# Optimization experiments

Hardware: AMD Instinct MI355X
Metric: run time of the kernel (lower is better)

Reference implementation:

```python
import jax, jax.numpy as jnp
import numpy as np


def setup_inputs() -> dict:
    key = jax.random.key(0)
    k1, k2, k3, k4, k5 = jax.random.split(key, 5)
    B, S, I, N = 64, 512, 2, 2048
    scale = (1.0 / N) ** 0.5
    velocities = jax.random.normal(k1, (B, S, I), dtype=jnp.float32)
    h0 = jax.random.uniform(k2, (B, N), dtype=jnp.float32)
    W_lin = jax.random.normal(k3, (N, I), dtype=jnp.float32) * scale
    b_lin = jax.random.normal(k4, (N,), dtype=jnp.float32) * scale
    W_rec = jax.random.normal(k5, (N, N), dtype=jnp.float32) * scale
    return {"velocities": velocities, "h0": h0, "W_lin": W_lin,
            "b_lin": b_lin, "W_rec": W_rec}


def reference(velocities, h0, W_lin, b_lin, W_rec):
    # velocities: [B, S, 2]; h0: [B, N]; W_lin: [N, 2]; b_lin: [N]; W_rec: [N, N]
    # base_logits = Linear(velocities): [B, S, N]
    base_logits = jnp.einsum('bsi,ni->bsn', velocities, W_lin) + b_lin

    def step(h, logits_t):
        # logits_t: [B, N]; h: [B, N] (probabilities)
        z = logits_t + h @ W_rec
        h_new = jax.nn.softmax(z, axis=-1)
        return h_new, h_new

    # scan over time axis S
    _, outs = jax.lax.scan(step, h0, jnp.swapaxes(base_logits, 0, 1))
    # outs: [S, B, N] -> [B, S, N]
    return jnp.swapaxes(outs, 0, 1)
```

## Files before the change

### kernel.cpp

```cpp
#include <hip/hip_runtime.h>
#include <stdint.h>

typedef __attribute__((ext_vector_type(8))) short short8;
typedef __attribute__((ext_vector_type(4))) float floatx4;

static constexpr int kB = 64, kS = 512, kN = 2048;

static constexpr size_t CTR_OFF        = 0;
static constexpr size_t CTR_BYTES      = 4 * 513 * 4;
static constexpr size_t RSP_OFF        = 16384;
static constexpr size_t RSP_BYTES_BIG  = (size_t)kS * 4 * 16 * 64 * 4;
static constexpr size_t RSP_BYTES_SM   = (size_t)2 * 4 * 16 * 64 * 4;
static constexpr size_t SLAB           = (size_t)kB * kN * 2;
static constexpr size_t EBUF_OFF_BIG   = RSP_OFF + RSP_BYTES_BIG;
static constexpr size_t TOTAL_BIG      = EBUF_OFF_BIG + 513 * SLAB;
static constexpr size_t EBUF_OFF_SM    = RSP_OFF + RSP_BYTES_SM;
static constexpr size_t TOTAL_SM       = EBUF_OFF_SM + 2 * SLAB;

__device__ __forceinline__ unsigned short f2bf(float x) {
    unsigned u = __builtin_bit_cast(unsigned, x);
    u = (u + 0x7fffu + ((u >> 16) & 1u)) >> 16;
    return (unsigned short)u;
}

__device__ __forceinline__ void domain_barrier(unsigned* slot, unsigned count) {
    __syncthreads();
    if (threadIdx.x == 0) {
        __hip_atomic_fetch_add(slot, 1u, __ATOMIC_RELAXED, __HIP_MEMORY_SCOPE_AGENT);
        while (__hip_atomic_load(slot, __ATOMIC_RELAXED, __HIP_MEMORY_SCOPE_AGENT) < count)
            __builtin_amdgcn_s_sleep(1);
    }
    __syncthreads();
}

struct ULL2 { unsigned long long lo, hi; };

template<bool BIG>
__global__ __launch_bounds__(256) void pcn(
    const float* __restrict__ vel, const float* __restrict__ h0,
    const float* __restrict__ Wlin, const float* __restrict__ blin,
    const float* __restrict__ Wrec, float* __restrict__ out,
    float* rsp, unsigned* ctr, unsigned short* ebuf)
{
    extern __shared__ char smem[];
    short8* Wlds = (short8*)smem;
    float*  red  = (float*)(smem + 131072);

    const int tid  = threadIdx.x;
    const int lane = tid & 63;
    const int w    = tid >> 6;
    const int bg   = (blockIdx.x & 7) >> 1;
    const int cg   = ((blockIdx.x >> 3) << 1) | (blockIdx.x & 1);
    const int b0   = bg * 16;
    const int c0   = cg * 32;
    const int koff = (lane >> 4) << 3;

    for (int kt = w * 16; kt < w * 16 + 16; ++kt) {
        for (int ct = 0; ct < 2; ++ct) {
            const int colg = c0 + ct * 16 + (lane & 15);
            const int kb   = kt * 32 + koff;
            short8 v;
            #pragma unroll
            for (int j = 0; j < 8; ++j)
                v[j] = (short)f2bf(Wrec[(size_t)(kb + j) * kN + colg]);
            Wlds[(kt * 2 + ct) * 64 + lane] = v;
        }
    }

    const int r   = tid >> 4;
    const int c16 = tid & 15;
    const int cc  = c16 * 2;

    {
        const float a0 = h0[(size_t)(b0 + r) * kN + c0 + cc];
        const float a1 = h0[(size_t)(b0 + r) * kN + c0 + cc + 1];
        const unsigned pk = (unsigned)f2bf(a0) | ((unsigned)f2bf(a1) << 16);
        __hip_atomic_store((unsigned*)(ebuf + (size_t)(b0 + r) * kN + c0 + cc), pk,
                           __ATOMIC_RELAXED, __HIP_MEMORY_SCOPE_AGENT);
    }

    const float wl00 = Wlin[(c0 + cc) * 2 + 0],     wl01 = Wlin[(c0 + cc) * 2 + 1];
    const float wl10 = Wlin[(c0 + cc + 1) * 2 + 0], wl11 = Wlin[(c0 + cc + 1) * 2 + 1];
    const float bl0  = blin[c0 + cc], bl1 = blin[c0 + cc + 1];

    domain_barrier(ctr + bg * 513 + 512, 64);

    float s_inv = 1.0f;
    float ep0 = 0.0f, ep1 = 0.0f;
    const int arow = b0 + (lane & 15);

    for (int t = 0; t < kS; ++t) {
        const int rslot = BIG ? t       : (t & 1);
        const int wslot = BIG ? (t + 1) : ((t + 1) & 1);
        const unsigned short* ebR = ebuf + (size_t)rslot * (kB * kN);

        floatx4 acc0 = {0.f,0.f,0.f,0.f}, acc1 = {0.f,0.f,0.f,0.f};
        #pragma unroll
        for (int kt = 0; kt < 16; ++kt) {
            const int ktg = w * 16 + kt;
            const unsigned short* ap = ebR + (size_t)arow * kN + ktg * 32 + koff;
            short8 a;
            if (BIG) {
                a = *(const short8*)ap;
            } else {
                ULL2 u;
                u.lo = __hip_atomic_load((const unsigned long long*)ap,
                                         __ATOMIC_RELAXED, __HIP_MEMORY_SCOPE_AGENT);
                u.hi = __hip_atomic_load((const unsigned long long*)ap + 1,
                                         __ATOMIC_RELAXED, __HIP_MEMORY_SCOPE_AGENT);
                a = __builtin_bit_cast(short8, u);
            }
            const short8 bq0 = Wlds[(ktg * 2 + 0) * 64 + lane];
            const short8 bq1 = Wlds[(ktg * 2 + 1) * 64 + lane];
            acc0 = __builtin_amdgcn_mfma_f32_16x16x32_bf16(a, bq0, acc0, 0, 0, 0);
            acc1 = __builtin_amdgcn_mfma_f32_16x16x32_bf16(a, bq1, acc1, 0, 0, 0);
        }
        {
            const int ccol = lane & 15, crow = (lane >> 4) * 4;
            #pragma unroll
            for (int i = 0; i < 4; ++i) {
                red[w * 512 + (crow + i) * 32 + ccol]      = acc0[i];
                red[w * 512 + (crow + i) * 32 + 16 + ccol] = acc1[i];
            }
        }
        __syncthreads();
        float g0 = 0.f, g1 = 0.f;
        {
            const int cell = tid * 2;
            #pragma unroll
            for (int ww = 0; ww < 4; ++ww) {
                g0 += red[ww * 512 + cell];
                g1 += red[ww * 512 + cell + 1];
            }
        }

        const float v0 = vel[((size_t)(b0 + r) * kS + t) * 2 + 0];
        const float v1 = vel[((size_t)(b0 + r) * kS + t) * 2 + 1];
        const float z0 = fmaf(g0, s_inv, fmaf(v0, wl00, fmaf(v1, wl01, bl0)));
        const float z1 = fmaf(g1, s_inv, fmaf(v0, wl10, fmaf(v1, wl11, bl1)));
        const float e0 = __expf(z0), e1 = __expf(z1);

        float es = e0 + e1;
        es += __shfl_xor(es, 8, 16);
        es += __shfl_xor(es, 4, 16);
        es += __shfl_xor(es, 2, 16);
        es += __shfl_xor(es, 1, 16);
        if (c16 == 0) {
            const size_t pidx = (((size_t)rslot * 4 + bg) * 16 + r) * 64 + cg;
            __hip_atomic_store(rsp + pidx, es, __ATOMIC_RELAXED, __HIP_MEMORY_SCOPE_AGENT);
        }

        {
            const unsigned pk = (unsigned)f2bf(e0) | ((unsigned)f2bf(e1) << 16);
            __hip_atomic_store(
                (unsigned*)(ebuf + (size_t)wslot * (kB * kN) + (size_t)(b0 + r) * kN + c0 + cc),
                pk, __ATOMIC_RELAXED, __HIP_MEMORY_SCOPE_AGENT);
        }

        if (t > 0) {
            float2 o; o.x = ep0 * s_inv; o.y = ep1 * s_inv;
            *(float2*)(out + ((size_t)(b0 + r) * kS + (t - 1)) * kN + c0 + cc) = o;
        }
        ep0 = e0; ep1 = e1;

        domain_barrier(ctr + bg * 513 + t, 64);

        {
            const float* rp = rsp + (((size_t)rslot * 4 + bg) * 16 + r) * 64 + c16 * 4;
            float s;
            if (BIG) {
                const floatx4 v = *(const floatx4*)rp;
                s = (v[0] + v[1]) + (v[2] + v[3]);
            } else {
                float p0 = __hip_atomic_load(rp + 0, __ATOMIC_RELAXED, __HIP_MEMORY_SCOPE_AGENT);
                float p1 = __hip_atomic_load(rp + 1, __ATOMIC_RELAXED, __HIP_MEMORY_SCOPE_AGENT);
                float p2 = __hip_atomic_load(rp + 2, __ATOMIC_RELAXED, __HIP_MEMORY_SCOPE_AGENT);
                float p3 = __hip_atomic_load(rp + 3, __ATOMIC_RELAXED, __HIP_MEMORY_SCOPE_AGENT);
                s = (p0 + p1) + (p2 + p3);
            }
            s += __shfl_xor(s, 8, 16);
            s += __shfl_xor(s, 4, 16);
            s += __shfl_xor(s, 2, 16);
            s += __shfl_xor(s, 1, 16);
            s_inv = 1.0f / s;
        }
    }
    {
        float2 o; o.x = ep0 * s_inv; o.y = ep1 * s_inv;
        *(float2*)(out + ((size_t)(b0 + r) * kS + (kS - 1)) * kN + c0 + cc) = o;
    }
}

extern "C" void kernel_launch(void* const* d_in, const int* in_sizes, int n_in,
                              void* d_out, int out_size, void* d_ws, size_t ws_size,
                              hipStream_t stream)
{
    (void)in_sizes; (void)n_in; (void)out_size;
    const float* vel  = (const float*)d_in[0];
    const float* h0   = (const float*)d_in[1];
    const float* Wlin = (const float*)d_in[2];
    const float* blin = (const float*)d_in[3];
    const float* Wrec = (const float*)d_in[4];
    float* out = (float*)d_out;

    char* ws = (char*)d_ws;
    unsigned* ctr = (unsigned*)(ws + CTR_OFF);
    const bool big = ws_size >= TOTAL_BIG;
    float* rsp            = (float*)(ws + RSP_OFF);
    unsigned short* ebuf  = (unsigned short*)(ws + (big ? EBUF_OFF_BIG : EBUF_OFF_SM));

    (void)hipMemsetAsync(ws + CTR_OFF, 0, CTR_BYTES, stream);

    const unsigned smem = 131072 + 8192;
    const void* fn = big ? (const void*)pcn<true> : (const void*)pcn<false>;
    (void)hipFuncSetAttribute(fn, hipFuncAttributeMaxDynamicSharedMemorySize, (int)smem);

    void* args[] = { (void*)&vel, (void*)&h0, (void*)&Wlin, (void*)&blin,
                     (void*)&Wrec, (void*)&out, (void*)&rsp, (void*)&ctr, (void*)&ebuf };
    hipError_t err = hipLaunchCooperativeKernel(fn, dim3(256), dim3(256), args, smem, stream);
    if (err != hipSuccess) {
        (void)hipGetLastError();
        if (big)
            hipLaunchKernelGGL(pcn<true>, dim3(256), dim3(256), smem, stream,
                               vel, h0, Wlin, blin, Wrec, out, rsp, ctr, ebuf);
        else
            hipLaunchKernelGGL(pcn<false>, dim3(256), dim3(256), smem, stream,
                               vel, h0, Wlin, blin, Wrec, out, rsp, ctr, ebuf);
    }
}
```

Measured before the change: 2.716 ms.

## Replace counter barrier with per-block flagged partial sums and a ring buffer

Drops the atomic counter barrier (fetch-add followed by a single-thread spin) and instead has each block publish its nonzero partial softmax sum as a flag. Every thread polls all 64 partials directly, which merges synchronisation and the normaliser reduction into one step. The exp buffer becomes a 4-slot ring, all A-fragment loads are issued before the MFMA loop, and each step's output is written in the same iteration instead of one step later. The risks are more polling traffic from all threads, correctness that depends on relaxed ordering between the ebuf stores and the flag stores, and a zero-sum flag being read as not ready.

```diff
diff --git a/kernel.cpp b/kernel.cpp
--- a/kernel.cpp
+++ b/kernel.cpp
@@ -5,17 +5,12 @@
 typedef __attribute__((ext_vector_type(4))) float floatx4;
 
 static constexpr int kB = 64, kS = 512, kN = 2048;
-
-static constexpr size_t CTR_OFF        = 0;
-static constexpr size_t CTR_BYTES      = 4 * 513 * 4;
-static constexpr size_t RSP_OFF        = 16384;
-static constexpr size_t RSP_BYTES_BIG  = (size_t)kS * 4 * 16 * 64 * 4;
-static constexpr size_t RSP_BYTES_SM   = (size_t)2 * 4 * 16 * 64 * 4;
-static constexpr size_t SLAB           = (size_t)kB * kN * 2;
-static constexpr size_t EBUF_OFF_BIG   = RSP_OFF + RSP_BYTES_BIG;
-static constexpr size_t TOTAL_BIG      = EBUF_OFF_BIG + 513 * SLAB;
-static constexpr size_t EBUF_OFF_SM    = RSP_OFF + RSP_BYTES_SM;
-static constexpr size_t TOTAL_SM       = EBUF_OFF_SM + 2 * SLAB;
+static constexpr int RING = 4;
+
+static constexpr size_t FLG_OFF    = 0;
+static constexpr size_t FLG_BYTES  = (size_t)(kS + 1) * 4 * 64 * 16 * 4;
+static constexpr size_t EBUF_OFF   = (FLG_BYTES + 4095) & ~(size_t)4095;
+static constexpr size_t SLAB_ELEMS = (size_t)kB * kN;
 
 __device__ __forceinline__ unsigned short f2bf(float x) {
     unsigned u = __builtin_bit_cast(unsigned, x);
@@ -23,24 +18,13 @@
     return (unsigned short)u;
 }
 
-__device__ __forceinline__ void domain_barrier(unsigned* slot, unsigned count) {
-    __syncthreads();
-    if (threadIdx.x == 0) {
-        __hip_atomic_fetch_add(slot, 1u, __ATOMIC_RELAXED, __HIP_MEMORY_SCOPE_AGENT);
-        while (__hip_atomic_load(slot, __ATOMIC_RELAXED, __HIP_MEMORY_SCOPE_AGENT) < count)
-            __builtin_amdgcn_s_sleep(1);
-    }
-    __syncthreads();
-}
-
 struct ULL2 { unsigned long long lo, hi; };
 
-template<bool BIG>
 __global__ __launch_bounds__(256) void pcn(
     const float* __restrict__ vel, const float* __restrict__ h0,
     const float* __restrict__ Wlin, const float* __restrict__ blin,
     const float* __restrict__ Wrec, float* __restrict__ out,
-    float* rsp, unsigned* ctr, unsigned short* ebuf)
+    float* flg, unsigned short* ebuf)
 {
     extern __shared__ char smem[];
     short8* Wlds = (short8*)smem;
@@ -83,33 +67,43 @@
     const float wl10 = Wlin[(c0 + cc + 1) * 2 + 0], wl11 = Wlin[(c0 + cc + 1) * 2 + 1];
     const float bl0  = blin[c0 + cc], bl1 = blin[c0 + cc + 1];
 
-    domain_barrier(ctr + bg * 513 + 512, 64);
+    __syncthreads();
+    if (c16 == 0)
+        __hip_atomic_store(flg + (((size_t)kS * 4 + bg) * 64 + cg) * 16 + r, 1.0f,
+                           __ATOMIC_RELAXED, __HIP_MEMORY_SCOPE_AGENT);
+    {
+        const float* fpb = flg + ((size_t)kS * 4 + bg) * 64 * 16 + r;
+        bool rdy = false;
+        do {
+            const float p0 = __hip_atomic_load(fpb + (c16 * 4 + 0) * 16, __ATOMIC_RELAXED, __HIP_MEMORY_SCOPE_AGENT);
+            const float p1 = __hip_atomic_load(fpb + (c16 * 4 + 1) * 16, __ATOMIC_RELAXED, __HIP_MEMORY_SCOPE_AGENT);
+            const float p2 = __hip_atomic_load(fpb + (c16 * 4 + 2) * 16, __ATOMIC_RELAXED, __HIP_MEMORY_SCOPE_AGENT);
+            const float p3 = __hip_atomic_load(fpb + (c16 * 4 + 3) * 16, __ATOMIC_RELAXED, __HIP_MEMORY_SCOPE_AGENT);
+            rdy = (p0 != 0.f) & (p1 != 0.f) & (p2 != 0.f) & (p3 != 0.f);
+        } while (!__all((int)rdy));
+    }
 
     float s_inv = 1.0f;
-    float ep0 = 0.0f, ep1 = 0.0f;
     const int arow = b0 + (lane & 15);
 
     for (int t = 0; t < kS; ++t) {
-        const int rslot = BIG ? t       : (t & 1);
-        const int wslot = BIG ? (t + 1) : ((t + 1) & 1);
-        const unsigned short* ebR = ebuf + (size_t)rslot * (kB * kN);
-
+        const float2 vv = *(const float2*)(vel + ((size_t)(b0 + r) * kS + t) * 2);
+
+        const unsigned short* ebR = ebuf + (size_t)(t % RING) * SLAB_ELEMS;
+        ULL2 afrag[16];
+        #pragma unroll
+        for (int kt = 0; kt < 16; ++kt) {
+            const int ktg = w * 16 + kt;
+            const unsigned long long* ap =
+                (const unsigned long long*)(ebR + (size_t)arow * kN + ktg * 32 + koff);
+            afrag[kt].lo = __hip_atomic_load(ap,     __ATOMIC_RELAXED, __HIP_MEMORY_SCOPE_AGENT);
+            afrag[kt].hi = __hip_atomic_load(ap + 1, __ATOMIC_RELAXED, __HIP_MEMORY_SCOPE_AGENT);
+        }
         floatx4 acc0 = {0.f,0.f,0.f,0.f}, acc1 = {0.f,0.f,0.f,0.f};
         #pragma unroll
         for (int kt = 0; kt < 16; ++kt) {
             const int ktg = w * 16 + kt;
-            const unsigned short* ap = ebR + (size_t)arow * kN + ktg * 32 + koff;
-            short8 a;
-            if (BIG) {
-                a = *(const short8*)ap;
-            } else {
-                ULL2 u;
-                u.lo = __hip_atomic_load((const unsigned long long*)ap,
-                                         __ATOMIC_RELAXED, __HIP_MEMORY_SCOPE_AGENT);
-                u.hi = __hip_atomic_load((const unsigned long long*)ap + 1,
-                                         __ATOMIC_RELAXED, __HIP_MEMORY_SCOPE_AGENT);
-                a = __builtin_bit_cast(short8, u);
-            }
+            const short8 a   = __builtin_bit_cast(short8, afrag[kt]);
             const short8 bq0 = Wlds[(ktg * 2 + 0) * 64 + lane];
             const short8 bq1 = Wlds[(ktg * 2 + 1) * 64 + lane];
             acc0 = __builtin_amdgcn_mfma_f32_16x16x32_bf16(a, bq0, acc0, 0, 0, 0);
@@ -134,10 +128,8 @@
             }
         }
 
-        const float v0 = vel[((size_t)(b0 + r) * kS + t) * 2 + 0];
-        const float v1 = vel[((size_t)(b0 + r) * kS + t) * 2 + 1];
-        const float z0 = fmaf(g0, s_inv, fmaf(v0, wl00, fmaf(v1, wl01, bl0)));
-        const float z1 = fmaf(g1, s_inv, fmaf(v0, wl10, fmaf(v1, wl11, bl1)));
+        const float z0 = fmaf(g0, s_inv, fmaf(vv.x, wl00, fmaf(vv.y, wl01, bl0)));
+        const float z1 = fmaf(g1, s_inv, fmaf(vv.x, wl10, fmaf(vv.y, wl11, bl1)));
         const float e0 = __expf(z0), e1 = __expf(z1);
 
         float es = e0 + e1;
@@ -145,49 +137,44 @@
         es += __shfl_xor(es, 4, 16);
         es += __shfl_xor(es, 2, 16);
         es += __shfl_xor(es, 1, 16);
-        if (c16 == 0) {
-            const size_t pidx = (((size_t)rslot * 4 + bg) * 16 + r) * 64 + cg;
-            __hip_atomic_store(rsp + pidx, es, __ATOMIC_RELAXED, __HIP_MEMORY_SCOPE_AGENT);
-        }
 
         {
             const unsigned pk = (unsigned)f2bf(e0) | ((unsigned)f2bf(e1) << 16);
             __hip_atomic_store(
-                (unsigned*)(ebuf + (size_t)wslot * (kB * kN) + (size_t)(b0 + r) * kN + c0 + cc),
+                (unsigned*)(ebuf + (size_t)((t + 1) % RING) * SLAB_ELEMS
+                            + (size_t)(b0 + r) * kN + c0 + cc),
                 pk, __ATOMIC_RELAXED, __HIP_MEMORY_SCOPE_AGENT);
         }
 
-        if (t > 0) {
-            float2 o; o.x = ep0 * s_inv; o.y = ep1 * s_inv;
-            *(float2*)(out + ((size_t)(b0 + r) * kS + (t - 1)) * kN + c0 + cc) = o;
-        }
-        ep0 = e0; ep1 = e1;
-
-        domain_barrier(ctr + bg * 513 + t, 64);
-
-        {
-            const float* rp = rsp + (((size_t)rslot * 4 + bg) * 16 + r) * 64 + c16 * 4;
-            float s;
-            if (BIG) {
-                const floatx4 v = *(const floatx4*)rp;
-                s = (v[0] + v[1]) + (v[2] + v[3]);
-            } else {
-                float p0 = __hip_atomic_load(rp + 0, __ATOMIC_RELAXED, __HIP_MEMORY_SCOPE_AGENT);
-                float p1 = __hip_atomic_load(rp + 1, __ATOMIC_RELAXED, __HIP_MEMORY_SCOPE_AGENT);
-                float p2 = __hip_atomic_load(rp + 2, __ATOMIC_RELAXED, __HIP_MEMORY_SCOPE_AGENT);
-                float p3 = __hip_atomic_load(rp + 3, __ATOMIC_RELAXED, __HIP_MEMORY_SCOPE_AGENT);
-                s = (p0 + p1) + (p2 + p3);
-            }
-            s += __shfl_xor(s, 8, 16);
-            s += __shfl_xor(s, 4, 16);
-            s += __shfl_xor(s, 2, 16);
-            s += __shfl_xor(s, 1, 16);
-            s_inv = 1.0f / s;
-        }
-    }
-    {
-        float2 o; o.x = ep0 * s_inv; o.y = ep1 * s_inv;
-        *(float2*)(out + ((size_t)(b0 + r) * kS + (kS - 1)) * kN + c0 + cc) = o;
+        __syncthreads();
+
+        if (c16 == 0)
+            __hip_atomic_store(flg + (((size_t)t * 4 + bg) * 64 + cg) * 16 + r, es,
+                               __ATOMIC_RELAXED, __HIP_MEMORY_SCOPE_AGENT);
+
+        float p0, p1, p2, p3;
+        {
+            const float* fpb = flg + ((size_t)t * 4 + bg) * 64 * 16 + r;
+            bool rdy = false;
+            do {
+                p0 = __hip_atomic_load(fpb + (c16 * 4 + 0) * 16, __ATOMIC_RELAXED, __HIP_MEMORY_SCOPE_AGENT);
+                p1 = __hip_atomic_load(fpb + (c16 * 4 + 1) * 16, __ATOMIC_RELAXED, __HIP_MEMORY_SCOPE_AGENT);
+                p2 = __hip_atomic_load(fpb + (c16 * 4 + 2) * 16, __ATOMIC_RELAXED, __HIP_MEMORY_SCOPE_AGENT);
+                p3 = __hip_atomic_load(fpb + (c16 * 4 + 3) * 16, __ATOMIC_RELAXED, __HIP_MEMORY_SCOPE_AGENT);
+                rdy = (p0 != 0.f) & (p1 != 0.f) & (p2 != 0.f) & (p3 != 0.f);
+            } while (!__all((int)rdy));
+        }
+        float s = (p0 + p1) + (p2 + p3);
+        s += __shfl_xor(s, 8, 16);
+        s += __shfl_xor(s, 4, 16);
+        s += __shfl_xor(s, 2, 16);
+        s += __shfl_xor(s, 1, 16);
+        s_inv = 1.0f / s;
+
+        {
+            float2 o; o.x = e0 * s_inv; o.y = e1 * s_inv;
+            *(float2*)(out + ((size_t)(b0 + r) * kS + t) * kN + c0 + cc) = o;
+        }
     }
 }
 
@@ -195,7 +182,7 @@
                               void* d_out, int out_size, void* d_ws, size_t ws_size,
                               hipStream_t stream)
 {
-    (void)in_sizes; (void)n_in; (void)out_size;
+    (void)in_sizes; (void)n_in; (void)out_size; (void)ws_size;
     const float* vel  = (const float*)d_in[0];
     const float* h0   = (const float*)d_in[1];
     const float* Wlin = (const float*)d_in[2];
@@ -204,27 +191,22 @@
     float* out = (float*)d_out;
 
     char* ws = (char*)d_ws;
-    unsigned* ctr = (unsigned*)(ws + CTR_OFF);
-    const bool big = ws_size >= TOTAL_BIG;
-    float* rsp            = (float*)(ws + RSP_OFF);
-    unsigned short* ebuf  = (unsigned short*)(ws + (big ? EBUF_OFF_BIG : EBUF_OFF_SM));
-
-    (void)hipMemsetAsync(ws + CTR_OFF, 0, CTR_BYTES, stream);
+    float* flg           = (float*)(ws + FLG_OFF);
+    unsigned short* ebuf = (unsigned short*)(ws + EBUF_OFF);
+
+    (void)hipMemsetAsync(ws + FLG_OFF, 0, FLG_BYTES, stream);
 
     const unsigned smem = 131072 + 8192;
-    const void* fn = big ? (const void*)pcn<true> : (const void*)pcn<false>;
-    (void)hipFuncSetAttribute(fn, hipFuncAttributeMaxDynamicSharedMemorySize, (int)smem);
+    (void)hipFuncSetAttribute((const void*)pcn,
+        hipFuncAttributeMaxDynamicSharedMemorySize, (int)smem);
 
     void* args[] = { (void*)&vel, (void*)&h0, (void*)&Wlin, (void*)&blin,
-                     (void*)&Wrec, (void*)&out, (void*)&rsp, (void*)&ctr, (void*)&ebuf };
-    hipError_t err = hipLaunchCooperativeKernel(fn, dim3(256), dim3(256), args, smem, stream);
+                     (void*)&Wrec, (void*)&out, (void*)&flg, (void*)&ebuf };
+    hipError_t err = hipLaunchCooperativeKernel((const void*)pcn,
+        dim3(256), dim3(256), args, smem, stream);
     if (err != hipSuccess) {
         (void)hipGetLastError();
-        if (big)
-            hipLaunchKernelGGL(pcn<true>, dim3(256), dim3(256), smem, stream,
-                               vel, h0, Wlin, blin, Wrec, out, rsp, ctr, ebuf);
-        else
-            hipLaunchKernelGGL(pcn<false>, dim3(256), dim3(256), smem, stream,
-                               vel, h0, Wlin, blin, Wrec, out, rsp, ctr, ebuf);
+        hipLaunchKernelGGL(pcn, dim3(256), dim3(256), smem, stream,
+                           vel, h0, Wlin, blin, Wrec, out, flg, ebuf);
     }
 }
```

Measured after the change: 3.531 ms. +30.0%, slower.
